# Optimization experiments

Measured on AMD Instinct MI355X. Metric: run time of the kernel, lower is better.

## Reference

```python
import jax, jax.numpy as jnp
import numpy as np


def setup_inputs() -> dict:
    key = jax.random.key(0)
    ks = jax.random.split(key, 8)
    B, N, D, E, S = 8, 4096, 1024, 64, 2
    H = D
    T = E * S  # total slots = 128
    return {
        "x": jax.random.normal(ks[0], (B, N, D), jnp.float32),
        "phi_w": jax.random.normal(ks[1], (T, D), jnp.float32) * 0.02,
        "fc1_w": jax.random.normal(ks[2], (E, H, D), jnp.float32) * 0.02,
        "fc1_b": jax.random.normal(ks[3], (E, H), jnp.float32) * 0.02,
        "fc2_w": jax.random.normal(ks[4], (E, D, H), jnp.float32) * 0.02,
        "fc2_b": jax.random.normal(ks[5], (E, D), jnp.float32) * 0.02,
        "out_w": jax.random.normal(ks[6], (D, D), jnp.float32) * 0.02,
        "out_b": jax.random.normal(ks[7], (D,), jnp.float32) * 0.02,
    }


def reference(x, phi_w, fc1_w, fc1_b, fc2_w, fc2_b, out_w, out_b):
    B, N, D = x.shape
    E, H, _ = fc1_w.shape
    T = phi_w.shape[0]
    S = T // E
    # dispatch logits: (B, N, T)
    logits = jnp.einsum('bnd,td->bnt', x, phi_w)
    dispatch_w = jax.nn.softmax(logits, axis=1)  # softmax over tokens
    combine_w = jax.nn.softmax(logits, axis=2)   # softmax over slots
    # dispatch: compress tokens -> slots, (B, T, D) -> (B, E, S, D)
    slots = jnp.einsum('bnt,bnd->btd', dispatch_w, x).reshape(B, E, S, D)
    # per-expert tiny MLP (no weight duplication over B)
    h = jnp.einsum('besd,ehd->besh', slots, fc1_w) + fc1_b[None, :, None, :]
    h = jax.nn.gelu(h, approximate=True)  # tanh approximation, matches torch
    out = jnp.einsum('besh,edh->besd', h, fc2_w) + fc2_b[None, :, None, :]
    out = out.reshape(B, T, D)
    # combine: expand slots -> tokens
    combined = jnp.einsum('bnt,btd->bnd', combine_w, out)
    output = jnp.einsum('bnd,od->bno', combined, out_w) + out_b
    aux_loss = jnp.asarray(0.0, dtype=x.dtype)
    return output, aux_loss
```

## Files before the change

### kernel.cpp

```cpp
#include <hip/hip_runtime.h>
#include <math.h>

#define B_ 8
#define N_ 4096
#define D_ 1024
#define E_ 64
#define T_ 128

using bf16   = __bf16;
using bf16x4 = __attribute__((ext_vector_type(4))) __bf16;
using bf16x8 = __attribute__((ext_vector_type(8))) __bf16;
using f32x4  = __attribute__((ext_vector_type(4))) float;

#define MFMA16(a, b, c) __builtin_amdgcn_mfma_f32_16x16x32_bf16(a, b, c, 0, 0, 0)
#define LDK 72

__device__ __forceinline__ bf16x8 ldsfrag(const bf16* p) {
  const int lane = threadIdx.x & 63;
  return *(const bf16x8*)(p + (lane & 15) * LDK + (lane >> 4) * 8);
}

__device__ __forceinline__ bf16x8 cvt8(float4 a, float4 b) {
  return (bf16x8){(bf16)a.x, (bf16)a.y, (bf16)a.z, (bf16)a.w,
                  (bf16)b.x, (bf16)b.y, (bf16)b.z, (bf16)b.w};
}

__global__ void k_convert(const float* __restrict__ phi, const float* __restrict__ ow,
                          bf16* __restrict__ phi_bf, bf16* __restrict__ ow_bf)
{
  if (blockIdx.x < 128) {
    int i = blockIdx.x * 256 + threadIdx.x;
    float4 v = ((const float4*)phi)[i];
    ((bf16x4*)phi_bf)[i] = (bf16x4){(bf16)v.x, (bf16)v.y, (bf16)v.z, (bf16)v.w};
  } else {
    int i = (blockIdx.x - 128) * 256 + threadIdx.x;
    float4 v = ((const float4*)ow)[i];
    ((bf16x4*)ow_bf)[i] = (bf16x4){(bf16)v.x, (bf16)v.y, (bf16)v.z, (bf16)v.w};
  }
}

__global__ __launch_bounds__(256) void k_logits(
    const float* __restrict__ X, const bf16* __restrict__ Phi,
    float* __restrict__ L, bf16* __restrict__ Xbf, bf16* __restrict__ CW,
    float* __restrict__ redM, float* __restrict__ redS)
{
  __shared__ __align__(16) char smraw[34048];
  bf16 (*As)[LDK] = (bf16(*)[LDK])smraw;
  bf16 (*Bs)[LDK] = (bf16(*)[LDK])(smraw + 64 * LDK * 2);
  float (*S)[133] = (float(*)[133])smraw;

  const int m0 = blockIdx.x * 64;
  const int tid = threadIdx.x;
  const int wave = tid >> 6, lane = tid & 63;
  const int wm = (wave >> 1) * 32;
  const int wn = (wave & 1) * 64;

  f32x4 acc[2][4];
#pragma unroll
  for (int i = 0; i < 2; ++i)
#pragma unroll
    for (int j = 0; j < 4; ++j) acc[i][j] = (f32x4){0.f, 0.f, 0.f, 0.f};

  const int ar = tid >> 2, ac = (tid & 3) * 16;
  const int br = tid >> 1, bc = (tid & 1) * 32;

  for (int k0 = 0; k0 < 1024; k0 += 64) {
    const float* xp = X + (long)(m0 + ar) * 1024 + k0 + ac;
    float4 v0 = *(const float4*)(xp + 0);
    float4 v1 = *(const float4*)(xp + 4);
    float4 v2 = *(const float4*)(xp + 8);
    float4 v3 = *(const float4*)(xp + 12);
    bf16x8 p0 = cvt8(v0, v1);
    bf16x8 p1 = cvt8(v2, v3);
    *(bf16x8*)&As[ar][ac]     = p0;
    *(bf16x8*)&As[ar][ac + 8] = p1;
    bf16* xo = Xbf + (long)(m0 + ar) * 1024 + k0 + ac;
    *(bf16x8*)xo       = p0;
    *(bf16x8*)(xo + 8) = p1;

    const bf16* pp = Phi + (long)br * 1024 + k0 + bc;
    *(bf16x8*)&Bs[br][bc + 0]  = *(const bf16x8*)(pp + 0);
    *(bf16x8*)&Bs[br][bc + 8]  = *(const bf16x8*)(pp + 8);
    *(bf16x8*)&Bs[br][bc + 16] = *(const bf16x8*)(pp + 16);
    *(bf16x8*)&Bs[br][bc + 24] = *(const bf16x8*)(pp + 24);
    __syncthreads();
#pragma unroll
    for (int kk = 0; kk < 64; kk += 32) {
      bf16x8 a0 = ldsfrag(&As[wm][kk]);
      bf16x8 a1 = ldsfrag(&As[wm + 16][kk]);
#pragma unroll
      for (int n = 0; n < 4; ++n) {
        bf16x8 bb = ldsfrag(&Bs[wn + n * 16][kk]);
        acc[0][n] = MFMA16(a0, bb, acc[0][n]);
        acc[1][n] = MFMA16(a1, bb, acc[1][n]);
      }
    }
    __syncthreads();
  }
  const int cc = lane & 15, rr = (lane >> 4) * 4;
#pragma unroll
  for (int m = 0; m < 2; ++m)
#pragma unroll
    for (int n = 0; n < 4; ++n)
#pragma unroll
      for (int j = 0; j < 4; ++j) {
        const float val = acc[m][n][j];
        L[(long)(m0 + wm + m * 16 + rr + j) * 128 + wn + n * 16 + cc] = val;
        S[wm + m * 16 + rr + j][wn + n * 16 + cc] = val;
      }
  __syncthreads();

  const int r = tid >> 2, q = tid & 3;
  float v[32];
#pragma unroll
  for (int i = 0; i < 8; ++i)
#pragma unroll
    for (int j = 0; j < 4; ++j) v[i * 4 + j] = S[r][q * 4 + i * 16 + j];
  float mx = -1e30f;
#pragma unroll
  for (int i = 0; i < 32; ++i) mx = fmaxf(mx, v[i]);
  mx = fmaxf(mx, __shfl_xor(mx, 1));
  mx = fmaxf(mx, __shfl_xor(mx, 2));
  float sum = 0.f;
#pragma unroll
  for (int i = 0; i < 32; ++i) { v[i] = expf(v[i] - mx); sum += v[i]; }
  sum += __shfl_xor(sum, 1);
  sum += __shfl_xor(sum, 2);
  const float inv = 1.f / sum;
  bf16* cwr = CW + (long)(m0 + r) * 128 + q * 4;
#pragma unroll
  for (int i = 0; i < 8; ++i)
    *(bf16x4*)(cwr + i * 16) = (bf16x4){(bf16)(v[i*4+0]*inv), (bf16)(v[i*4+1]*inv),
                                        (bf16)(v[i*4+2]*inv), (bf16)(v[i*4+3]*inv)};

  if (tid < 128) {
    const int t = tid;
    float m = -1e30f, s = 0.f;
    for (int rj = 0; rj < 64; ++rj) {
      float val = S[rj][t];
      if (val > m) { s = s * expf(m - val) + 1.f; m = val; }
      else         { s += expf(val - m); }
    }
    const long chunk = m0 >> 6;
    redM[chunk * 128 + t] = m;
    redS[chunk * 128 + t] = s;
  }
}

__global__ void disp_final(const float* __restrict__ redM, const float* __restrict__ redS,
                           float* __restrict__ Mf, float* __restrict__ Zf)
{
  int idx = blockIdx.x * 256 + threadIdx.x;
  int b = idx >> 7, t = idx & 127;
  float m = -1e30f, s = 0.f;
  for (int c = 0; c < 64; ++c) {
    float mc = redM[((long)b * 64 + c) * 128 + t];
    float sc = redS[((long)b * 64 + c) * 128 + t];
    float nm = fmaxf(m, mc);
    s = s * expf(m - nm) + sc * expf(mc - nm);
    m = nm;
  }
  Mf[idx] = m;
  Zf[idx] = 1.f / s;
}

__global__ __launch_bounds__(256) void k_dwt(const float* __restrict__ L,
    const float* __restrict__ Mf, const float* __restrict__ Zf, bf16* __restrict__ DWT)
{
  __shared__ float S[64][132];
  const int b = blockIdx.y, n0 = blockIdx.x * 64;
  const int tid = threadIdx.x;
  const int r = tid >> 2;
  const int c0 = (tid & 3) * 32;
  const float* Lp = L + ((long)b * N_ + n0 + r) * T_ + c0;
#pragma unroll
  for (int i = 0; i < 32; i += 4) {
    float4 v = *(const float4*)(Lp + i);
    S[r][c0 + i + 0] = v.x;
    S[r][c0 + i + 1] = v.y;
    S[r][c0 + i + 2] = v.z;
    S[r][c0 + i + 3] = v.w;
  }
  __syncthreads();
  const int nc = (tid & 7) * 8;
  for (int ti = tid >> 3; ti < 128; ti += 32) {
    const float mf = Mf[b * 128 + ti], zf = Zf[b * 128 + ti];
    bf16x8 o;
#pragma unroll
    for (int j = 0; j < 8; ++j) o[j] = (bf16)(expf(S[nc + j][ti] - mf) * zf);
    *(bf16x8*)(DWT + ((long)b * 128 + ti) * 4096 + n0 + nc) = o;
  }
}

__global__ __launch_bounds__(256) void k_slots(
    const bf16* __restrict__ DWT, const bf16* __restrict__ Xbf, float* __restrict__ Part)
{
  __shared__ bf16 As[128][LDK];
  __shared__ bf16 Bs[128][LDK];
  const int b = blockIdx.z >> 3, chunk = blockIdx.z & 7;
  const int d0 = blockIdx.x * 128;
  const int tid = threadIdx.x, wave = tid >> 6, lane = tid & 63;
  const int wm = (wave >> 1) * 64, wn = (wave & 1) * 64;

  f32x4 acc[4][4];
#pragma unroll
  for (int i = 0; i < 4; ++i)
#pragma unroll
    for (int j = 0; j < 4; ++j) acc[i][j] = (f32x4){0.f, 0.f, 0.f, 0.f};

  const int at = tid >> 1, anc = (tid & 1) * 32;
  const int bn = tid >> 2, bdc = (tid & 3) * 32;
  const long dwt_b = (long)b * 128 * 4096;
  const long x_b   = (long)b * 4096 * 1024;

  for (int k0 = 0; k0 < 512; k0 += 64) {
    const int nbase = chunk * 512 + k0;
    const bf16* ap = DWT + dwt_b + (long)at * 4096 + nbase + anc;
    *(bf16x8*)&As[at][anc + 0]  = *(const bf16x8*)(ap + 0);
    *(bf16x8*)&As[at][anc + 8]  = *(const bf16x8*)(ap + 8);
    *(bf16x8*)&As[at][anc + 16] = *(const bf16x8*)(ap + 16);
    *(bf16x8*)&As[at][anc + 24] = *(const bf16x8*)(ap + 24);
    const bf16* xp = Xbf + x_b + (long)(nbase + bn) * 1024 + d0 + bdc;
    bf16x8 q0 = *(const bf16x8*)(xp + 0);
    bf16x8 q1 = *(const bf16x8*)(xp + 8);
    bf16x8 q2 = *(const bf16x8*)(xp + 16);
    bf16x8 q3 = *(const bf16x8*)(xp + 24);
#pragma unroll
    for (int i = 0; i < 8; ++i) {
      Bs[bdc + i][bn]      = q0[i];
      Bs[bdc + 8 + i][bn]  = q1[i];
      Bs[bdc + 16 + i][bn] = q2[i];
      Bs[bdc + 24 + i][bn] = q3[i];
    }
    __syncthreads();
#pragma unroll
    for (int kk = 0; kk < 64; kk += 32) {
      bf16x8 af[4], bfr[4];
#pragma unroll
      for (int m = 0; m < 4; ++m) af[m]  = ldsfrag(&As[wm + m * 16][kk]);
#pragma unroll
      for (int n = 0; n < 4; ++n) bfr[n] = ldsfrag(&Bs[wn + n * 16][kk]);
#pragma unroll
      for (int m = 0; m < 4; ++m)
#pragma unroll
        for (int n = 0; n < 4; ++n)
          acc[m][n] = MFMA16(af[m], bfr[n], acc[m][n]);
    }
    __syncthreads();
  }
  const int cc = lane & 15, rr = (lane >> 4) * 4;
  float* Cp = Part + ((long)chunk * 8 + b) * 128 * 1024;
#pragma unroll
  for (int m = 0; m < 4; ++m)
#pragma unroll
    for (int n = 0; n < 4; ++n)
#pragma unroll
      for (int j = 0; j < 4; ++j)
        Cp[(long)(wm + m * 16 + rr + j) * 1024 + d0 + wn + n * 16 + cc] = acc[m][n][j];
}

__global__ void k_reduce8(const float* __restrict__ P, bf16* __restrict__ O)
{
  long base = ((long)blockIdx.x * 256 + threadIdx.x) * 4;
  float4 s = *(const float4*)(P + base);
  for (int c = 1; c < 8; ++c) {
    float4 v = *(const float4*)(P + (long)c * 1048576 + base);
    s.x += v.x; s.y += v.y; s.z += v.z; s.w += v.w;
  }
  *(bf16x4*)(O + base) = (bf16x4){(bf16)s.x, (bf16)s.y, (bf16)s.z, (bf16)s.w};
}

template<int GELU, int INL>
__global__ __launch_bounds__(256) void k_expert(
    const bf16* __restrict__ Ab, const float* __restrict__ W,
    const float* __restrict__ bias, bf16* __restrict__ Out)
{
  __shared__ bf16 As[16][LDK];
  __shared__ bf16 Bs[64][LDK];
  const int e = blockIdx.y;
  const int h0 = blockIdx.x * 64;
  const int tid = threadIdx.x, wave = tid >> 6, lane = tid & 63;
  f32x4 acc = (f32x4){0.f, 0.f, 0.f, 0.f};

  const int hr = tid >> 2, kc = (tid & 3) * 16;

  for (int k0 = 0; k0 < 1024; k0 += 64) {
    if (tid < 128) {
      int r = tid >> 3, akc = (tid & 7) * 8;
      long row = (INL == 0) ? (long)((r >> 1) * 128 + e * 2 + (r & 1)) : (long)(e * 16 + r);
      *(bf16x8*)&As[r][akc] = *(const bf16x8*)(Ab + row * 1024 + k0 + akc);
    }
    const float* wp = W + ((long)e * 1024 + h0 + hr) * 1024 + k0 + kc;
    float4 w0 = *(const float4*)(wp + 0);
    float4 w1 = *(const float4*)(wp + 4);
    float4 w2 = *(const float4*)(wp + 8);
    float4 w3 = *(const float4*)(wp + 12);
    *(bf16x8*)&Bs[hr][kc]     = cvt8(w0, w1);
    *(bf16x8*)&Bs[hr][kc + 8] = cvt8(w2, w3);
    __syncthreads();
    bf16x8 a0 = ldsfrag(&As[0][0]);
    bf16x8 b0 = ldsfrag(&Bs[wave * 16][0]);
    acc = MFMA16(a0, b0, acc);
    a0 = ldsfrag(&As[0][32]);
    b0 = ldsfrag(&Bs[wave * 16][32]);
    acc = MFMA16(a0, b0, acc);
    __syncthreads();
  }
  const int cc = lane & 15, rr = (lane >> 4) * 4;
  const int h = h0 + wave * 16 + cc;
  const float bs = bias[e * 1024 + h];
#pragma unroll
  for (int j = 0; j < 4; ++j) {
    float v = acc[j] + bs;
    if (GELU) {
      float x3 = v * v * v;
      v = 0.5f * v * (1.f + tanhf(0.7978845608028654f * (v + 0.044715f * x3)));
    }
    int m = rr + j;
    long orow = (INL == 0) ? (long)(e * 16 + m) : (long)((m >> 1) * 128 + e * 2 + (m & 1));
    Out[orow * 1024 + h] = (bf16)v;
  }
}

__global__ __launch_bounds__(256) void k_proj(
    const bf16* __restrict__ OWbf, const bf16* __restrict__ OS, bf16* __restrict__ PT)
{
  __shared__ bf16 As[64][LDK];
  __shared__ bf16 Bs[64][LDK];
  const int o0 = blockIdx.y * 64, t0 = blockIdx.x * 64;
  const int tid = threadIdx.x, wave = tid >> 6, lane = tid & 63;
  const int wm = (wave >> 1) * 32, wn = (wave & 1) * 32;
  f32x4 acc[2][2];
#pragma unroll
  for (int i = 0; i < 2; ++i)
#pragma unroll
    for (int j = 0; j < 2; ++j) acc[i][j] = (f32x4){0.f, 0.f, 0.f, 0.f};

  const int r = tid >> 2, kc = (tid & 3) * 16;
  for (int k0 = 0; k0 < 1024; k0 += 64) {
    const bf16* apo = OWbf + (long)(o0 + r) * 1024 + k0 + kc;
    *(bf16x8*)&As[r][kc]     = *(const bf16x8*)(apo + 0);
    *(bf16x8*)&As[r][kc + 8] = *(const bf16x8*)(apo + 8);
    const bf16* bpo = OS + (long)(t0 + r) * 1024 + k0 + kc;
    *(bf16x8*)&Bs[r][kc]     = *(const bf16x8*)(bpo + 0);
    *(bf16x8*)&Bs[r][kc + 8] = *(const bf16x8*)(bpo + 8);
    __syncthreads();
#pragma unroll
    for (int kk = 0; kk < 64; kk += 32) {
      bf16x8 a0 = ldsfrag(&As[wm][kk]);
      bf16x8 a1 = ldsfrag(&As[wm + 16][kk]);
      bf16x8 b0 = ldsfrag(&Bs[wn][kk]);
      bf16x8 b1 = ldsfrag(&Bs[wn + 16][kk]);
      acc[0][0] = MFMA16(a0, b0, acc[0][0]);
      acc[0][1] = MFMA16(a0, b1, acc[0][1]);
      acc[1][0] = MFMA16(a1, b0, acc[1][0]);
      acc[1][1] = MFMA16(a1, b1, acc[1][1]);
    }
    __syncthreads();
  }
  const int cc = lane & 15, rr = (lane >> 4) * 4;
#pragma unroll
  for (int m = 0; m < 2; ++m)
#pragma unroll
    for (int n = 0; n < 2; ++n)
#pragma unroll
      for (int j = 0; j < 4; ++j)
        PT[(long)(o0 + wm + m * 16 + rr + j) * 1024 + t0 + wn + n * 16 + cc] =
            (bf16)acc[m][n][j];
}

__global__ __launch_bounds__(256) void k_combine(
    const bf16* __restrict__ CW, const bf16* __restrict__ PT,
    const float* __restrict__ ob, float* __restrict__ O)
{
  __shared__ bf16 As[128][LDK];
  __shared__ bf16 Bs[128][LDK];
  const int b = blockIdx.z, m0 = blockIdx.y * 128, o0 = blockIdx.x * 128;
  const int tid = threadIdx.x, wave = tid >> 6, lane = tid & 63;
  const int wm = (wave >> 1) * 64, wn = (wave & 1) * 64;

  if (blockIdx.x == 0 && blockIdx.y == 0 && blockIdx.z == 0 && tid == 0)
    O[(long)B_ * N_ * D_] = 0.f;

  f32x4 acc[4][4];
#pragma unroll
  for (int i = 0; i < 4; ++i)
#pragma unroll
    for (int j = 0; j < 4; ++j) acc[i][j] = (f32x4){0.f, 0.f, 0.f, 0.f};

  const int r = tid >> 1, tc = (tid & 1) * 32;
  for (int k0 = 0; k0 < 128; k0 += 64) {
    const bf16* ap = CW + ((long)b * N_ + m0 + r) * 128 + k0 + tc;
    *(bf16x8*)&As[r][tc + 0]  = *(const bf16x8*)(ap + 0);
    *(bf16x8*)&As[r][tc + 8]  = *(const bf16x8*)(ap + 8);
    *(bf16x8*)&As[r][tc + 16] = *(const bf16x8*)(ap + 16);
    *(bf16x8*)&As[r][tc + 24] = *(const bf16x8*)(ap + 24);
    const bf16* bp = PT + (long)(o0 + r) * 1024 + b * 128 + k0 + tc;
    *(bf16x8*)&Bs[r][tc + 0]  = *(const bf16x8*)(bp + 0);
    *(bf16x8*)&Bs[r][tc + 8]  = *(const bf16x8*)(bp + 8);
    *(bf16x8*)&Bs[r][tc + 16] = *(const bf16x8*)(bp + 16);
    *(bf16x8*)&Bs[r][tc + 24] = *(const bf16x8*)(bp + 24);
    __syncthreads();
#pragma unroll
    for (int kk = 0; kk < 64; kk += 32) {
      bf16x8 af[4], bfr[4];
#pragma unroll
      for (int m = 0; m < 4; ++m) af[m]  = ldsfrag(&As[wm + m * 16][kk]);
#pragma unroll
      for (int n = 0; n < 4; ++n) bfr[n] = ldsfrag(&Bs[wn + n * 16][kk]);
#pragma unroll
      for (int m = 0; m < 4; ++m)
#pragma unroll
        for (int n = 0; n < 4; ++n)
          acc[m][n] = MFMA16(af[m], bfr[n], acc[m][n]);
    }
    __syncthreads();
  }
  const int cc = lane & 15, rr = (lane >> 4) * 4;
#pragma unroll
  for (int n = 0; n < 4; ++n) {
    const int o = o0 + wn + n * 16 + cc;
    const float bv = ob[o];
#pragma unroll
    for (int m = 0; m < 4; ++m)
#pragma unroll
      for (int j = 0; j < 4; ++j)
        O[((long)b * N_ + m0 + wm + m * 16 + rr + j) * 1024 + o] = acc[m][n][j] + bv;
  }
}

extern "C" void kernel_launch(void* const* d_in, const int* in_sizes, int n_in,
                              void* d_out, int out_size, void* d_ws, size_t ws_size,
                              hipStream_t stream)
{
  const float* x     = (const float*)d_in[0];
  const float* phi_w = (const float*)d_in[1];
  const float* fc1_w = (const float*)d_in[2];
  const float* fc1_b = (const float*)d_in[3];
  const float* fc2_w = (const float*)d_in[4];
  const float* fc2_b = (const float*)d_in[5];
  const float* out_w = (const float*)d_in[6];
  const float* out_b = (const float*)d_in[7];
  float* out = (float*)d_out;

  float* ws     = (float*)d_ws;
  float* logits = ws;
  float* redM   = logits + 4194304;
  float* redS   = redM + 65536;
  float* Mf     = redS + 65536;
  float* Zf     = Mf + 1024;
  bf16* DWT     = (bf16*)(Zf + 1024);
  bf16* CW      = DWT + 4194304;
  bf16* slots   = CW + 4194304;
  bf16* hbuf    = slots + 1048576;
  bf16* outs    = hbuf + 1048576;
  bf16* projT   = outs + 1048576;
  bf16* phi_bf  = projT + 1048576;
  bf16* outw_bf = phi_bf + 131072;

  bf16* Xbf   = (bf16*)d_out;
  float* Part = (float*)d_out + 16777216;

  k_convert<<<dim3(1152), 256, 0, stream>>>(phi_w, out_w, phi_bf, outw_bf);
  k_logits<<<dim3(512), 256, 0, stream>>>(x, phi_bf, logits, Xbf, CW, redM, redS);
  disp_final<<<dim3(4), 256, 0, stream>>>(redM, redS, Mf, Zf);
  k_dwt<<<dim3(64, 8), 256, 0, stream>>>(logits, Mf, Zf, DWT);
  k_slots<<<dim3(8, 1, 64), 256, 0, stream>>>(DWT, Xbf, Part);
  k_reduce8<<<dim3(1024), 256, 0, stream>>>(Part, slots);
  k_expert<1, 0><<<dim3(16, 64), 256, 0, stream>>>(slots, fc1_w, fc1_b, hbuf);
  k_expert<0, 1><<<dim3(16, 64), 256, 0, stream>>>(hbuf, fc2_w, fc2_b, outs);
  k_proj<<<dim3(16, 16), 256, 0, stream>>>(outw_bf, outs, projT);
  k_combine<<<dim3(8, 32, 8), 256, 0, stream>>>(CW, projT, out_b, out);
}
```

Baseline: 325.6 us.

## Shrink logits tiles, fuse dispatch reductions into consumers, swizzle slots LDS

```diff
diff --git a/kernel.cpp b/kernel.cpp
--- a/kernel.cpp
+++ b/kernel.cpp
@@ -44,39 +44,32 @@
     float* __restrict__ L, bf16* __restrict__ Xbf, bf16* __restrict__ CW,
     float* __restrict__ redM, float* __restrict__ redS)
 {
-  __shared__ __align__(16) char smraw[34048];
+  __shared__ __align__(16) char smraw[23040];
   bf16 (*As)[LDK] = (bf16(*)[LDK])smraw;
-  bf16 (*Bs)[LDK] = (bf16(*)[LDK])(smraw + 64 * LDK * 2);
+  bf16 (*Bs)[LDK] = (bf16(*)[LDK])(smraw + 32 * LDK * 2);
   float (*S)[133] = (float(*)[133])smraw;
 
-  const int m0 = blockIdx.x * 64;
+  const int m0 = blockIdx.x * 32;
   const int tid = threadIdx.x;
   const int wave = tid >> 6, lane = tid & 63;
-  const int wm = (wave >> 1) * 32;
-  const int wn = (wave & 1) * 64;
-
-  f32x4 acc[2][4];
+  const int wn = wave * 32;
+
+  f32x4 acc[2][2];
 #pragma unroll
   for (int i = 0; i < 2; ++i)
 #pragma unroll
-    for (int j = 0; j < 4; ++j) acc[i][j] = (f32x4){0.f, 0.f, 0.f, 0.f};
-
-  const int ar = tid >> 2, ac = (tid & 3) * 16;
+    for (int j = 0; j < 2; ++j) acc[i][j] = (f32x4){0.f, 0.f, 0.f, 0.f};
+
+  const int ar = tid >> 3, ac = (tid & 7) * 8;
   const int br = tid >> 1, bc = (tid & 1) * 32;
 
   for (int k0 = 0; k0 < 1024; k0 += 64) {
     const float* xp = X + (long)(m0 + ar) * 1024 + k0 + ac;
     float4 v0 = *(const float4*)(xp + 0);
     float4 v1 = *(const float4*)(xp + 4);
-    float4 v2 = *(const float4*)(xp + 8);
-    float4 v3 = *(const float4*)(xp + 12);
     bf16x8 p0 = cvt8(v0, v1);
-    bf16x8 p1 = cvt8(v2, v3);
-    *(bf16x8*)&As[ar][ac]     = p0;
-    *(bf16x8*)&As[ar][ac + 8] = p1;
-    bf16* xo = Xbf + (long)(m0 + ar) * 1024 + k0 + ac;
-    *(bf16x8*)xo       = p0;
-    *(bf16x8*)(xo + 8) = p1;
+    *(bf16x8*)&As[ar][ac] = p0;
+    *(bf16x8*)(Xbf + (long)(m0 + ar) * 1024 + k0 + ac) = p0;
 
     const bf16* pp = Phi + (long)br * 1024 + k0 + bc;
     *(bf16x8*)&Bs[br][bc + 0]  = *(const bf16x8*)(pp + 0);
@@ -86,14 +79,14 @@
     __syncthreads();
 #pragma unroll
     for (int kk = 0; kk < 64; kk += 32) {
-      bf16x8 a0 = ldsfrag(&As[wm][kk]);
-      bf16x8 a1 = ldsfrag(&As[wm + 16][kk]);
-#pragma unroll
-      for (int n = 0; n < 4; ++n) {
-        bf16x8 bb = ldsfrag(&Bs[wn + n * 16][kk]);
-        acc[0][n] = MFMA16(a0, bb, acc[0][n]);
-        acc[1][n] = MFMA16(a1, bb, acc[1][n]);
-      }
+      bf16x8 a0 = ldsfrag(&As[0][kk]);
+      bf16x8 a1 = ldsfrag(&As[16][kk]);
+      bf16x8 b0 = ldsfrag(&Bs[wn][kk]);
+      bf16x8 b1 = ldsfrag(&Bs[wn + 16][kk]);
+      acc[0][0] = MFMA16(a0, b0, acc[0][0]);
+      acc[0][1] = MFMA16(a0, b1, acc[0][1]);
+      acc[1][0] = MFMA16(a1, b0, acc[1][0]);
+      acc[1][1] = MFMA16(a1, b1, acc[1][1]);
     }
     __syncthreads();
   }
@@ -101,75 +94,63 @@
 #pragma unroll
   for (int m = 0; m < 2; ++m)
 #pragma unroll
-    for (int n = 0; n < 4; ++n)
+    for (int n = 0; n < 2; ++n)
 #pragma unroll
       for (int j = 0; j < 4; ++j) {
+        const int row = m * 16 + rr + j, col = wn + n * 16 + cc;
         const float val = acc[m][n][j];
-        L[(long)(m0 + wm + m * 16 + rr + j) * 128 + wn + n * 16 + cc] = val;
-        S[wm + m * 16 + rr + j][wn + n * 16 + cc] = val;
+        L[(long)(m0 + row) * 128 + col] = val;
+        S[row][col] = val;
       }
   __syncthreads();
 
-  const int r = tid >> 2, q = tid & 3;
-  float v[32];
-#pragma unroll
-  for (int i = 0; i < 8; ++i)
-#pragma unroll
-    for (int j = 0; j < 4; ++j) v[i * 4 + j] = S[r][q * 4 + i * 16 + j];
+  const int r = tid >> 3, q = tid & 7;
+  float v[16];
+#pragma unroll
+  for (int i = 0; i < 4; ++i)
+#pragma unroll
+    for (int j = 0; j < 4; ++j) v[i * 4 + j] = S[r][q * 4 + i * 32 + j];
   float mx = -1e30f;
 #pragma unroll
-  for (int i = 0; i < 32; ++i) mx = fmaxf(mx, v[i]);
+  for (int i = 0; i < 16; ++i) mx = fmaxf(mx, v[i]);
   mx = fmaxf(mx, __shfl_xor(mx, 1));
   mx = fmaxf(mx, __shfl_xor(mx, 2));
+  mx = fmaxf(mx, __shfl_xor(mx, 4));
   float sum = 0.f;
 #pragma unroll
-  for (int i = 0; i < 32; ++i) { v[i] = expf(v[i] - mx); sum += v[i]; }
+  for (int i = 0; i < 16; ++i) { v[i] = expf(v[i] - mx); sum += v[i]; }
   sum += __shfl_xor(sum, 1);
   sum += __shfl_xor(sum, 2);
+  sum += __shfl_xor(sum, 4);
   const float inv = 1.f / sum;
   bf16* cwr = CW + (long)(m0 + r) * 128 + q * 4;
 #pragma unroll
-  for (int i = 0; i < 8; ++i)
-    *(bf16x4*)(cwr + i * 16) = (bf16x4){(bf16)(v[i*4+0]*inv), (bf16)(v[i*4+1]*inv),
+  for (int i = 0; i < 4; ++i)
+    *(bf16x4*)(cwr + i * 32) = (bf16x4){(bf16)(v[i*4+0]*inv), (bf16)(v[i*4+1]*inv),
                                         (bf16)(v[i*4+2]*inv), (bf16)(v[i*4+3]*inv)};
 
   if (tid < 128) {
     const int t = tid;
     float m = -1e30f, s = 0.f;
-    for (int rj = 0; rj < 64; ++rj) {
+    for (int rj = 0; rj < 32; ++rj) {
       float val = S[rj][t];
       if (val > m) { s = s * expf(m - val) + 1.f; m = val; }
       else         { s += expf(val - m); }
     }
-    const long chunk = m0 >> 6;
-    redM[chunk * 128 + t] = m;
-    redS[chunk * 128 + t] = s;
-  }
-}
-
-__global__ void disp_final(const float* __restrict__ redM, const float* __restrict__ redS,
-                           float* __restrict__ Mf, float* __restrict__ Zf)
-{
-  int idx = blockIdx.x * 256 + threadIdx.x;
-  int b = idx >> 7, t = idx & 127;
-  float m = -1e30f, s = 0.f;
-  for (int c = 0; c < 64; ++c) {
-    float mc = redM[((long)b * 64 + c) * 128 + t];
-    float sc = redS[((long)b * 64 + c) * 128 + t];
-    float nm = fmaxf(m, mc);
-    s = s * expf(m - nm) + sc * expf(mc - nm);
-    m = nm;
-  }
-  Mf[idx] = m;
-  Zf[idx] = 1.f / s;
+    redM[(long)blockIdx.x * 128 + t] = m;
+    redS[(long)blockIdx.x * 128 + t] = s;
+  }
 }
 
 __global__ __launch_bounds__(256) void k_dwt(const float* __restrict__ L,
-    const float* __restrict__ Mf, const float* __restrict__ Zf, bf16* __restrict__ DWT)
+    const float* __restrict__ redM, const float* __restrict__ redS,
+    bf16* __restrict__ DWT)
 {
   __shared__ float S[64][132];
+  __shared__ float sMf[128], sZf[128];
   const int b = blockIdx.y, n0 = blockIdx.x * 64;
   const int tid = threadIdx.x;
+
   const int r = tid >> 2;
   const int c0 = (tid & 3) * 32;
   const float* Lp = L + ((long)b * N_ + n0 + r) * T_ + c0;
@@ -181,15 +162,35 @@
     S[r][c0 + i + 2] = v.z;
     S[r][c0 + i + 3] = v.w;
   }
+  if (tid < 128) {
+    const int t = tid;
+    float m = -1e30f, s = 0.f;
+    for (int c = 0; c < 128; ++c) {
+      float mc = redM[((long)b * 128 + c) * 128 + t];
+      float sc = redS[((long)b * 128 + c) * 128 + t];
+      float nm = fmaxf(m, mc);
+      s = s * expf(m - nm) + sc * expf(mc - nm);
+      m = nm;
+    }
+    sMf[t] = m;
+    sZf[t] = 1.f / s;
+  }
   __syncthreads();
   const int nc = (tid & 7) * 8;
   for (int ti = tid >> 3; ti < 128; ti += 32) {
-    const float mf = Mf[b * 128 + ti], zf = Zf[b * 128 + ti];
+    const float mf = sMf[ti], zf = sZf[ti];
     bf16x8 o;
 #pragma unroll
     for (int j = 0; j < 8; ++j) o[j] = (bf16)(expf(S[nc + j][ti] - mf) * zf);
     *(bf16x8*)(DWT + ((long)b * 128 + ti) * 4096 + n0 + nc) = o;
   }
+}
+
+__device__ __forceinline__ bf16x8 ldsfragB(const bf16 (*Bs)[LDK], int dbase, int kk) {
+  const int l = threadIdx.x & 63;
+  const int d = dbase + (l & 15);
+  const int c = ((l >> 4) * 8 + kk) ^ (((d >> 5) & 3) << 4);
+  return *(const bf16x8*)(&Bs[d][c]);
 }
 
 __global__ __launch_bounds__(256) void k_slots(
@@ -209,7 +210,8 @@
     for (int j = 0; j < 4; ++j) acc[i][j] = (f32x4){0.f, 0.f, 0.f, 0.f};
 
   const int at = tid >> 1, anc = (tid & 1) * 32;
-  const int bn = tid >> 2, bdc = (tid & 3) * 32;
+  const int bn = tid >> 2, bq = tid & 3, bdc = bq * 32;
+  const int bcol = bn ^ (bq << 4);
   const long dwt_b = (long)b * 128 * 4096;
   const long x_b   = (long)b * 4096 * 1024;
 
@@ -227,10 +229,10 @@
     bf16x8 q3 = *(const bf16x8*)(xp + 24);
 #pragma unroll
     for (int i = 0; i < 8; ++i) {
-      Bs[bdc + i][bn]      = q0[i];
-      Bs[bdc + 8 + i][bn]  = q1[i];
-      Bs[bdc + 16 + i][bn] = q2[i];
-      Bs[bdc + 24 + i][bn] = q3[i];
+      Bs[bdc + i][bcol]      = q0[i];
+      Bs[bdc + 8 + i][bcol]  = q1[i];
+      Bs[bdc + 16 + i][bcol] = q2[i];
+      Bs[bdc + 24 + i][bcol] = q3[i];
     }
     __syncthreads();
 #pragma unroll
@@ -239,7 +241,7 @@
 #pragma unroll
       for (int m = 0; m < 4; ++m) af[m]  = ldsfrag(&As[wm + m * 16][kk]);
 #pragma unroll
-      for (int n = 0; n < 4; ++n) bfr[n] = ldsfrag(&Bs[wn + n * 16][kk]);
+      for (int n = 0; n < 4; ++n) bfr[n] = ldsfragB(Bs, wn + n * 16, kk);
 #pragma unroll
       for (int m = 0; m < 4; ++m)
 #pragma unroll
@@ -259,20 +261,8 @@
         Cp[(long)(wm + m * 16 + rr + j) * 1024 + d0 + wn + n * 16 + cc] = acc[m][n][j];
 }
 
-__global__ void k_reduce8(const float* __restrict__ P, bf16* __restrict__ O)
-{
-  long base = ((long)blockIdx.x * 256 + threadIdx.x) * 4;
-  float4 s = *(const float4*)(P + base);
-  for (int c = 1; c < 8; ++c) {
-    float4 v = *(const float4*)(P + (long)c * 1048576 + base);
-    s.x += v.x; s.y += v.y; s.z += v.z; s.w += v.w;
-  }
-  *(bf16x4*)(O + base) = (bf16x4){(bf16)s.x, (bf16)s.y, (bf16)s.z, (bf16)s.w};
-}
-
-template<int GELU, int INL>
-__global__ __launch_bounds__(256) void k_expert(
-    const bf16* __restrict__ Ab, const float* __restrict__ W,
+__global__ __launch_bounds__(256) void k_fc1(
+    const float* __restrict__ Part, const float* __restrict__ W,
     const float* __restrict__ bias, bf16* __restrict__ Out)
 {
   __shared__ bf16 As[16][LDK];
@@ -283,13 +273,18 @@
   f32x4 acc = (f32x4){0.f, 0.f, 0.f, 0.f};
 
   const int hr = tid >> 2, kc = (tid & 3) * 16;
+  const int arr = tid >> 4, akq = (tid & 15) * 4;
+  const long arow = ((long)(arr >> 1) * 128 + e * 2 + (arr & 1)) * 1024;
 
   for (int k0 = 0; k0 < 1024; k0 += 64) {
-    if (tid < 128) {
-      int r = tid >> 3, akc = (tid & 7) * 8;
-      long row = (INL == 0) ? (long)((r >> 1) * 128 + e * 2 + (r & 1)) : (long)(e * 16 + r);
-      *(bf16x8*)&As[r][akc] = *(const bf16x8*)(Ab + row * 1024 + k0 + akc);
-    }
+    float4 s0 = *(const float4*)(Part + arow + k0 + akq);
+#pragma unroll
+    for (int c = 1; c < 8; ++c) {
+      float4 v = *(const float4*)(Part + (long)c * 1048576 + arow + k0 + akq);
+      s0.x += v.x; s0.y += v.y; s0.z += v.z; s0.w += v.w;
+    }
+    *(bf16x4*)&As[arr][akq] = (bf16x4){(bf16)s0.x, (bf16)s0.y, (bf16)s0.z, (bf16)s0.w};
+
     const float* wp = W + ((long)e * 1024 + h0 + hr) * 1024 + k0 + kc;
     float4 w0 = *(const float4*)(wp + 0);
     float4 w1 = *(const float4*)(wp + 4);
@@ -312,13 +307,53 @@
 #pragma unroll
   for (int j = 0; j < 4; ++j) {
     float v = acc[j] + bs;
-    if (GELU) {
-      float x3 = v * v * v;
-      v = 0.5f * v * (1.f + tanhf(0.7978845608028654f * (v + 0.044715f * x3)));
-    }
+    float x3 = v * v * v;
+    v = 0.5f * v * (1.f + tanhf(0.7978845608028654f * (v + 0.044715f * x3)));
+    Out[(long)(e * 16 + rr + j) * 1024 + h] = (bf16)v;
+  }
+}
+
+__global__ __launch_bounds__(256) void k_fc2(
+    const bf16* __restrict__ Ab, const float* __restrict__ W,
+    const float* __restrict__ bias, bf16* __restrict__ Out)
+{
+  __shared__ bf16 As[16][LDK];
+  __shared__ bf16 Bs[64][LDK];
+  const int e = blockIdx.y;
+  const int h0 = blockIdx.x * 64;
+  const int tid = threadIdx.x, wave = tid >> 6, lane = tid & 63;
+  f32x4 acc = (f32x4){0.f, 0.f, 0.f, 0.f};
+
+  const int hr = tid >> 2, kc = (tid & 3) * 16;
+
+  for (int k0 = 0; k0 < 1024; k0 += 64) {
+    if (tid < 128) {
+      int r = tid >> 3, akc = (tid & 7) * 8;
+      *(bf16x8*)&As[r][akc] = *(const bf16x8*)(Ab + (long)(e * 16 + r) * 1024 + k0 + akc);
+    }
+    const float* wp = W + ((long)e * 1024 + h0 + hr) * 1024 + k0 + kc;
+    float4 w0 = *(const float4*)(wp + 0);
+    float4 w1 = *(const float4*)(wp + 4);
+    float4 w2 = *(const float4*)(wp + 8);
+    float4 w3 = *(const float4*)(wp + 12);
+    *(bf16x8*)&Bs[hr][kc]     = cvt8(w0, w1);
+    *(bf16x8*)&Bs[hr][kc + 8] = cvt8(w2, w3);
+    __syncthreads();
+    bf16x8 a0 = ldsfrag(&As[0][0]);
+    bf16x8 b0 = ldsfrag(&Bs[wave * 16][0]);
+    acc = MFMA16(a0, b0, acc);
+    a0 = ldsfrag(&As[0][32]);
+    b0 = ldsfrag(&Bs[wave * 16][32]);
+    acc = MFMA16(a0, b0, acc);
+    __syncthreads();
+  }
+  const int cc = lane & 15, rr = (lane >> 4) * 4;
+  const int h = h0 + wave * 16 + cc;
+  const float bs = bias[e * 1024 + h];
+#pragma unroll
+  for (int j = 0; j < 4; ++j) {
     int m = rr + j;
-    long orow = (INL == 0) ? (long)(e * 16 + m) : (long)((m >> 1) * 128 + e * 2 + (m & 1));
-    Out[orow * 1024 + h] = (bf16)v;
+    Out[(long)((m >> 1) * 128 + e * 2 + (m & 1)) * 1024 + h] = (bf16)(acc[j] + bs);
   }
 }
 
@@ -446,13 +481,10 @@
   float* ws     = (float*)d_ws;
   float* logits = ws;
   float* redM   = logits + 4194304;
-  float* redS   = redM + 65536;
-  float* Mf     = redS + 65536;
-  float* Zf     = Mf + 1024;
-  bf16* DWT     = (bf16*)(Zf + 1024);
+  float* redS   = redM + 131072;
+  bf16* DWT     = (bf16*)(redS + 131072);
   bf16* CW      = DWT + 4194304;
-  bf16* slots   = CW + 4194304;
-  bf16* hbuf    = slots + 1048576;
+  bf16* hbuf    = CW + 4194304;
   bf16* outs    = hbuf + 1048576;
   bf16* projT   = outs + 1048576;
   bf16* phi_bf  = projT + 1048576;
@@ -462,13 +494,11 @@
   float* Part = (float*)d_out + 16777216;
 
   k_convert<<<dim3(1152), 256, 0, stream>>>(phi_w, out_w, phi_bf, outw_bf);
-  k_logits<<<dim3(512), 256, 0, stream>>>(x, phi_bf, logits, Xbf, CW, redM, redS);
-  disp_final<<<dim3(4), 256, 0, stream>>>(redM, redS, Mf, Zf);
-  k_dwt<<<dim3(64, 8), 256, 0, stream>>>(logits, Mf, Zf, DWT);
+  k_logits<<<dim3(1024), 256, 0, stream>>>(x, phi_bf, logits, Xbf, CW, redM, redS);
+  k_dwt<<<dim3(64, 8), 256, 0, stream>>>(logits, redM, redS, DWT);
   k_slots<<<dim3(8, 1, 64), 256, 0, stream>>>(DWT, Xbf, Part);
-  k_reduce8<<<dim3(1024), 256, 0, stream>>>(Part, slots);
-  k_expert<1, 0><<<dim3(16, 64), 256, 0, stream>>>(slots, fc1_w, fc1_b, hbuf);
-  k_expert<0, 1><<<dim3(16, 64), 256, 0, stream>>>(hbuf, fc2_w, fc2_b, outs);
+  k_fc1<<<dim3(16, 64), 256, 0, stream>>>(Part, fc1_w, fc1_b, hbuf);
+  k_fc2<<<dim3(16, 64), 256, 0, stream>>>(hbuf, fc2_w, fc2_b, outs);
   k_proj<<<dim3(16, 16), 256, 0, stream>>>(outw_bf, outs, projT);
   k_combine<<<dim3(8, 32, 8), 256, 0, stream>>>(CW, projT, out_b, out);
 }
```

Result: slower. 352.5 us (+8.3%).
